# Kernel optimization log

Hardware: AMD Instinct MI355X
Metric: run time of the kernel (lower is better)

The kernel has to match this reference:

```python
import jax, jax.numpy as jnp
import numpy as np

WIN = 9
EPS = 1e-05


def _box3d(x, win=WIN):
    """Sum over a win^3 box (zero-padded), equivalent to conv3d with a ones kernel.
    Implemented as three separable 1D convolutions (exact same math, O(win)/voxel)."""
    pad = win // 2
    for axis in range(3):  # spatial axes D, H, W
        kshape = [1, 1, 1, 1, 1]
        kshape[2 + axis] = win
        kern = jnp.ones(kshape, x.dtype)
        pads = [(0, 0)] * 3
        pads[axis] = (pad, pad)
        dn = jax.lax.conv_dimension_numbers(x.shape, kern.shape, ('NCDHW', 'OIDHW', 'NCDHW'))
        x = jax.lax.conv_general_dilated(x, kern, window_strides=(1, 1, 1),
                                         padding=pads, dimension_numbers=dn)
    return x


def setup_inputs() -> dict:
    key = jax.random.key(0)
    k1, k2 = jax.random.split(key)
    shape = (1, 1, 160, 192, 224)  # [N, C, D, H, W] brain-MRI-scale volume
    I = jax.random.normal(k1, shape, dtype=jnp.float32)
    J = jax.random.normal(k2, shape, dtype=jnp.float32)
    return {"I": I, "J": J}


def reference(I, J):
    win_size = WIN ** 3
    I2 = I * I
    J2 = J * J
    IJ = I * J
    I_sum = _box3d(I)
    J_sum = _box3d(J)
    I2_sum = _box3d(I2)
    J2_sum = _box3d(J2)
    IJ_sum = _box3d(IJ)
    u_I = I_sum / win_size
    u_J = J_sum / win_size
    cross = IJ_sum - u_J * I_sum - u_I * J_sum + u_I * u_J * win_size
    I_var = I2_sum - 2 * u_I * I_sum + u_I * u_I * win_size
    J_var = J2_sum - 2 * u_J * J_sum + u_J * u_J * win_size
    cc = cross * cross / (I_var * J_var + EPS)
    return -1.0 * jnp.mean(cc)
```

## Files before the change

### kernel.cpp

```cpp
#include <hip/hip_runtime.h>


#define DD 160
#define HH 192
#define WW 224
#define W4 56
#define SLICE (HH * WW)
#define NVOX (DD * SLICE)
#define TW 32
#define TH 16
#define EXTH 24
#define DCH 10
#define NTHR 512
#define SW_RS 33
#define SW_CS (EXTH * SW_RS)
#define SH_RS 33
#define SH_CS (TH * SH_RS)
#define EPS 1e-5f
#define INV_WSUM (1.0f / 729.0f)

__global__ __launch_bounds__(NTHR, 4) void ncc_fused(const float* __restrict__ I,
                                                     const float* __restrict__ J,
                                                     float* __restrict__ out) {
    __shared__ float SW[5 * SW_CS];
    __shared__ float SH[5 * SH_CS];
    __shared__ float wred[NTHR / 64];

    const int tid = threadIdx.x;
    const int tx = tid & 31, ty = tid >> 5;
    const int wlo = blockIdx.x * TW;
    const int hlo = blockIdx.y * TH;
    const int dlo = blockIdx.z * DCH;

    const int wr = tid >> 3;
    const int wc = tid & 7;
    const int gh = hlo - 4 + wr;
    const bool hok = (gh >= 0) && (gh < HH);
    const int gf0 = (wlo >> 2) - 1 + wc;

    const int hcol = tid & 31;
    const int hch = tid >> 5;

    const float4* Iv = (const float4*)I;
    const float4* Jv = (const float4*)J;

    float q0[9], q1[9], q2[9], q3[9], q4[9];
    #pragma unroll
    for (int k = 0; k < 9; ++k) { q0[k]=0.f; q1[k]=0.f; q2[k]=0.f; q3[k]=0.f; q4[k]=0.f; }
    float r0=0.f, r1=0.f, r2=0.f, r3=0.f, r4=0.f;
    float acc = 0.f;

    #pragma unroll 1
    for (int g = 0; g < 2; ++g) {
        #pragma unroll
        for (int ph = 0; ph < 9; ++ph) {
            const int i = g * 9 + ph;
            const int z = dlo - 4 + i;
            const bool valid = (z >= 0) && (z < DD);

            if (valid && tid < 192) {
                const int rowb = z * (SLICE / 4) + gh * W4;
                float ax[12], bx[12];
                #pragma unroll
                for (int k = 0; k < 3; ++k) {
                    const int f = gf0 + k;
                    float4 a = make_float4(0.f, 0.f, 0.f, 0.f);
                    float4 b = make_float4(0.f, 0.f, 0.f, 0.f);
                    if (hok && f >= 0 && f < W4) { a = Iv[rowb + f]; b = Jv[rowb + f]; }
                    ax[4*k] = a.x; ax[4*k+1] = a.y; ax[4*k+2] = a.z; ax[4*k+3] = a.w;
                    bx[4*k] = b.x; bx[4*k+1] = b.y; bx[4*k+2] = b.z; bx[4*k+3] = b.w;
                }
                float p2[12], p3[12], p4[12];
                #pragma unroll
                for (int k = 0; k < 12; ++k) {
                    p2[k] = ax[k] * ax[k];
                    p3[k] = bx[k] * bx[k];
                    p4[k] = ax[k] * bx[k];
                }
                float* wp = SW + wr * SW_RS + 4 * wc;
                auto emitch = [&](const float* v, float* o) {
                    float s = v[0];
                    #pragma unroll
                    for (int k = 1; k < 9; ++k) s += v[k];
                    o[0] = s;
                    s += v[9]  - v[0]; o[1] = s;
                    s += v[10] - v[1]; o[2] = s;
                    s += v[11] - v[2]; o[3] = s;
                };
                emitch(ax, wp);
                emitch(bx, wp + SW_CS);
                emitch(p2, wp + 2 * SW_CS);
                emitch(p3, wp + 3 * SW_CS);
                emitch(p4, wp + 4 * SW_CS);
            }
            __syncthreads();

            if (valid && tid < 160) {
                const float* p = SW + hch * SW_CS + hcol;
                float v[24];
                #pragma unroll
                for (int r = 0; r < 24; ++r) v[r] = p[r * SW_RS];
                float s = v[0];
                #pragma unroll
                for (int r = 1; r < 9; ++r) s += v[r];
                float* o = SH + hch * SH_CS + hcol;
                o[0] = s;
                #pragma unroll
                for (int r = 1; r < 16; ++r) {
                    s += v[r + 8] - v[r - 1];
                    o[r * SH_RS] = s;
                }
            }
            __syncthreads();

            float w0=0.f, w1=0.f, w2=0.f, w3=0.f, w4=0.f;
            if (valid) {
                const float* p = SH + ty * SH_RS + tx;
                w0 = p[0];
                w1 = p[SH_CS];
                w2 = p[2 * SH_CS];
                w3 = p[3 * SH_CS];
                w4 = p[4 * SH_CS];
            }
            r0 += w0 - q0[ph]; q0[ph] = w0;
            r1 += w1 - q1[ph]; q1[ph] = w1;
            r2 += w2 - q2[ph]; q2[ph] = w2;
            r3 += w3 - q3[ph]; q3[ph] = w3;
            r4 += w4 - q4[ph]; q4[ph] = w4;

            if (i >= 8) {
                float cross = r4 - r0 * r1 * INV_WSUM;
                float iv    = r2 - r0 * r0 * INV_WSUM;
                float jv    = r3 - r1 * r1 * INV_WSUM;
                acc += cross * cross * __builtin_amdgcn_rcpf(iv * jv + EPS);
            }
        }
    }

    #pragma unroll
    for (int off = 32; off > 0; off >>= 1) acc += __shfl_down(acc, off, 64);
    if ((tid & 63) == 0) wred[tid >> 6] = acc;
    __syncthreads();
    if (tid == 0) {
        float t = 0.f;
        #pragma unroll
        for (int k = 0; k < NTHR / 64; ++k) t += wred[k];
        atomicAdd(out, t * (-1.0f / (float)NVOX));
    }
}

extern "C" void kernel_launch(void* const* d_in, const int* in_sizes, int n_in,
                              void* d_out, int out_size, void* d_ws, size_t ws_size,
                              hipStream_t stream) {
    const float* I = (const float*)d_in[0];
    const float* J = (const float*)d_in[1];
    float* out = (float*)d_out;

    hipMemsetAsync(d_out, 0, sizeof(float), stream);

    dim3 blk(NTHR, 1, 1);
    dim3 grd(WW / TW, HH / TH, DD / DCH);
    ncc_fused<<<grd, blk, 0, stream>>>(I, J, out);
}
```

Before: 148.4 us.

## Double-buffer shared stages and overlap W-pass with H-pass across warps

Double-buffers the W-sum and H-sum shared buffers and splits the warps by role: threads 0-191 load and W-sum the next depth slice while threads 192-351 run the H-pass on the current slice. This takes one __syncthreads out of each depth step and overlaps global loads with the H-pass. The W-pass stores become float4 writes, with the row stride padded to 36 so they stay aligned. In exchange, shared memory roughly doubles, which may lower occupancy, and the H-pass now runs on fewer warps.

```diff
diff --git a/kernel.cpp b/kernel.cpp
--- a/kernel.cpp
+++ b/kernel.cpp
@@ -6,14 +6,14 @@
 #define WW 224
 #define W4 56
 #define SLICE (HH * WW)
+#define S4 (SLICE / 4)
 #define NVOX (DD * SLICE)
 #define TW 32
 #define TH 16
-#define EXTH 24
 #define DCH 10
 #define NTHR 512
-#define SW_RS 33
-#define SW_CS (EXTH * SW_RS)
+#define SW_RS 36
+#define SW_CS (24 * SW_RS)
 #define SH_RS 33
 #define SH_CS (TH * SH_RS)
 #define EPS 1e-5f
@@ -22,8 +22,8 @@
 __global__ __launch_bounds__(NTHR, 4) void ncc_fused(const float* __restrict__ I,
                                                      const float* __restrict__ J,
                                                      float* __restrict__ out) {
-    __shared__ float SW[5 * SW_CS];
-    __shared__ float SH[5 * SH_CS];
+    __shared__ float SW0[5 * SW_CS], SW1[5 * SW_CS];
+    __shared__ float SH0[5 * SH_CS], SH1[5 * SH_CS];
     __shared__ float wred[NTHR / 64];
 
     const int tid = threadIdx.x;
@@ -32,17 +32,51 @@
     const int hlo = blockIdx.y * TH;
     const int dlo = blockIdx.z * DCH;
 
-    const int wr = tid >> 3;
-    const int wc = tid & 7;
+    const int wr = tid >> 3, wc = tid & 7;
     const int gh = hlo - 4 + wr;
     const bool hok = (gh >= 0) && (gh < HH);
     const int gf0 = (wlo >> 2) - 1 + wc;
 
-    const int hcol = tid & 31;
-    const int hch = tid >> 5;
+    const int ht = tid - 192;
+    const int hcol = ht & 31, hch = ht >> 5;
 
     const float4* Iv = (const float4*)I;
     const float4* Jv = (const float4*)J;
+
+    auto w_stage = [&](int z, float* dst) {
+        const int rowb = z * S4 + gh * W4;
+        float ax[12], bx[12];
+        #pragma unroll
+        for (int k = 0; k < 3; ++k) {
+            const int f = gf0 + k;
+            float4 a = make_float4(0.f, 0.f, 0.f, 0.f);
+            float4 b = make_float4(0.f, 0.f, 0.f, 0.f);
+            if (hok && f >= 0 && f < W4) { a = Iv[rowb + f]; b = Jv[rowb + f]; }
+            ax[4*k] = a.x; ax[4*k+1] = a.y; ax[4*k+2] = a.z; ax[4*k+3] = a.w;
+            bx[4*k] = b.x; bx[4*k+1] = b.y; bx[4*k+2] = b.z; bx[4*k+3] = b.w;
+        }
+        float* wp = dst + wr * SW_RS + 4 * wc;
+        #pragma unroll
+        for (int ch = 0; ch < 5; ++ch) {
+            float v[12];
+            #pragma unroll
+            for (int k = 0; k < 12; ++k)
+                v[k] = (ch == 0) ? ax[k]
+                     : (ch == 1) ? bx[k]
+                     : (ch == 2) ? ax[k] * ax[k]
+                     : (ch == 3) ? bx[k] * bx[k]
+                     :             ax[k] * bx[k];
+            float s = v[0];
+            #pragma unroll
+            for (int k = 1; k < 9; ++k) s += v[k];
+            float4 o;
+            o.x = s;
+            s += v[9]  - v[0]; o.y = s;
+            s += v[10] - v[1]; o.z = s;
+            s += v[11] - v[2]; o.w = s;
+            *(float4*)(wp + ch * SW_CS) = o;
+        }
+    };
 
     float q0[9], q1[9], q2[9], q3[9], q4[9];
     #pragma unroll
@@ -50,60 +84,36 @@
     float r0=0.f, r1=0.f, r2=0.f, r3=0.f, r4=0.f;
     float acc = 0.f;
 
+    {
+        const int z0 = dlo - 4;
+        if (tid < 192 && z0 >= 0) w_stage(z0, SW0);
+    }
+    __syncthreads();
+
     #pragma unroll 1
     for (int g = 0; g < 2; ++g) {
         #pragma unroll
         for (int ph = 0; ph < 9; ++ph) {
             const int i = g * 9 + ph;
             const int z = dlo - 4 + i;
-            const bool valid = (z >= 0) && (z < DD);
+            const bool val = (z >= 0) && (z < DD);
+            const int par = (g + ph) & 1;
+            float* swR = par ? SW1 : SW0;
+            float* swW = par ? SW0 : SW1;
+            float* sh  = par ? SH1 : SH0;
 
-            if (valid && tid < 192) {
-                const int rowb = z * (SLICE / 4) + gh * W4;
-                float ax[12], bx[12];
-                #pragma unroll
-                for (int k = 0; k < 3; ++k) {
-                    const int f = gf0 + k;
-                    float4 a = make_float4(0.f, 0.f, 0.f, 0.f);
-                    float4 b = make_float4(0.f, 0.f, 0.f, 0.f);
-                    if (hok && f >= 0 && f < W4) { a = Iv[rowb + f]; b = Jv[rowb + f]; }
-                    ax[4*k] = a.x; ax[4*k+1] = a.y; ax[4*k+2] = a.z; ax[4*k+3] = a.w;
-                    bx[4*k] = b.x; bx[4*k+1] = b.y; bx[4*k+2] = b.z; bx[4*k+3] = b.w;
-                }
-                float p2[12], p3[12], p4[12];
-                #pragma unroll
-                for (int k = 0; k < 12; ++k) {
-                    p2[k] = ax[k] * ax[k];
-                    p3[k] = bx[k] * bx[k];
-                    p4[k] = ax[k] * bx[k];
-                }
-                float* wp = SW + wr * SW_RS + 4 * wc;
-                auto emitch = [&](const float* v, float* o) {
-                    float s = v[0];
-                    #pragma unroll
-                    for (int k = 1; k < 9; ++k) s += v[k];
-                    o[0] = s;
-                    s += v[9]  - v[0]; o[1] = s;
-                    s += v[10] - v[1]; o[2] = s;
-                    s += v[11] - v[2]; o[3] = s;
-                };
-                emitch(ax, wp);
-                emitch(bx, wp + SW_CS);
-                emitch(p2, wp + 2 * SW_CS);
-                emitch(p3, wp + 3 * SW_CS);
-                emitch(p4, wp + 4 * SW_CS);
-            }
-            __syncthreads();
-
-            if (valid && tid < 160) {
-                const float* p = SW + hch * SW_CS + hcol;
+            if (tid < 192) {
+                const int zn = z + 1;
+                if (i < DCH + 7 && zn >= 0 && zn < DD) w_stage(zn, swW);
+            } else if (ht < 160 && val) {
+                const float* p = swR + hch * SW_CS + hcol;
                 float v[24];
                 #pragma unroll
                 for (int r = 0; r < 24; ++r) v[r] = p[r * SW_RS];
                 float s = v[0];
                 #pragma unroll
                 for (int r = 1; r < 9; ++r) s += v[r];
-                float* o = SH + hch * SH_CS + hcol;
+                float* o = sh + hch * SH_CS + hcol;
                 o[0] = s;
                 #pragma unroll
                 for (int r = 1; r < 16; ++r) {
@@ -114,8 +124,8 @@
             __syncthreads();
 
             float w0=0.f, w1=0.f, w2=0.f, w3=0.f, w4=0.f;
-            if (valid) {
-                const float* p = SH + ty * SH_RS + tx;
+            if (val) {
+                const float* p = sh + ty * SH_RS + tx;
                 w0 = p[0];
                 w1 = p[SH_CS];
                 w2 = p[2 * SH_CS];
```

Result: faster. 140.6 us (-5.3%).
